# Performance work log

Hardware: AMD Instinct MI355X
Metric: run time of the kernel (lower is better)

Reference implementation:

```python
import jax, jax.numpy as jnp
import numpy as np


def mha(x, mask, wq, bq, wk, bk, wv, bv, wo, bo, n_heads):
    # Flaubert/XLM MultiHeadAttention (eval mode, dropout = identity).
    bs, qlen, dim = x.shape
    dph = dim // n_heads

    def split_heads(t):  # (bs, qlen, dim) -> (bs, n_heads, qlen, dph)
        return t.reshape(bs, qlen, n_heads, dph).transpose(0, 2, 1, 3)

    q = split_heads(x @ wq + bq) / jnp.sqrt(jnp.asarray(dph, x.dtype))
    k = split_heads(x @ wk + bk)
    v = split_heads(x @ wv + bv)

    scores = jnp.einsum('bhqd,bhkd->bhqk', q, k)  # (bs, h, qlen, klen)
    neg = jnp.finfo(scores.dtype).min
    scores = jnp.where((mask == 0)[:, None, None, :], neg, scores)
    weights = jax.nn.softmax(scores, axis=-1)
    ctx = jnp.einsum('bhqk,bhkd->bhqd', weights, v)
    ctx = ctx.transpose(0, 2, 1, 3).reshape(bs, qlen, dim)
    return ctx @ wo + bo


def setup_inputs() -> dict:
    key = jax.random.key(0)
    ks = jax.random.split(key, 20)
    bs, slen = 4, 1024
    d0, d1 = 192, 66
    std = 0.02
    inp = {
        'x': jax.random.normal(ks[0], (bs, slen, d0), jnp.float32),
        'y': jax.random.normal(ks[1], (bs, slen, d1), jnp.float32),
        'mask0': jax.random.randint(ks[2], (bs, slen), 0, 2, jnp.int32),
        'mask1': jax.random.randint(ks[3], (bs, slen), 0, 2, jnp.int32),
    }
    names0 = ['q0', 'k0', 'v0', 'o0']
    names1 = ['q1', 'k1', 'v1', 'o1']
    for i, n in enumerate(names0):
        inp[n + '_w'] = jax.random.normal(ks[4 + i], (d0, d0), jnp.float32) * std
        inp[n + '_b'] = jnp.zeros((d0,), jnp.float32)
    for i, n in enumerate(names1):
        inp[n + '_w'] = jax.random.normal(ks[8 + i], (d1, d1), jnp.float32) * std
        inp[n + '_b'] = jnp.zeros((d1,), jnp.float32)
    return inp


def reference(x, y, mask0, mask1,
              q0_w, q0_b, k0_w, k0_b, v0_w, v0_b, o0_w, o0_b,
              q1_w, q1_b, k1_w, k1_b, v1_w, v1_b, o1_w, o1_b):
    out0 = mha(x, mask0, q0_w, q0_b, k0_w, k0_b, v0_w, v0_b, o0_w, o0_b, n_heads=16)
    out1 = mha(y, mask1, q1_w, q1_b, k1_w, k1_b, v1_w, v1_b, o1_w, o1_b, n_heads=11)
    return (out0, out1)
```

## Files before the change

kernel.cpp:

```cpp
#include <hip/hip_runtime.h>
#include <math.h>


#define BS 4
#define SLEN 1024

#define Q0_OFF 0
#define C0_OFF 786432
#define Q1_OFF 1572864
#define C1_OFF 1843200
#define K0H_OFF 2113536
#define V0T_OFF 2506752
#define K1H_OFF 2899968
#define V1T_OFF 3080192

#define OUT0_SIZE 786432

#if __has_builtin(__builtin_amdgcn_exp2f)
#define EXP2(x) __builtin_amdgcn_exp2f(x)
#else
#define EXP2(x) __expf((x) * 0.69314718056f)
#endif

typedef _Float16 f16x2 __attribute__((ext_vector_type(2)));
typedef _Float16 f16x4 __attribute__((ext_vector_type(4)));
typedef _Float16 f16x8 __attribute__((ext_vector_type(8)));
typedef float f32x4 __attribute__((ext_vector_type(4)));

union F16x8U { f16x8 v8; f16x4 v4[2]; };

__device__ __forceinline__ void mfma_chunk(const _Float16* sA, const _Float16* sWT,
                                           int wv, int lane, f32x4 acc[4])
{
  const int col = lane & 15, grp = lane >> 4;
#pragma unroll
  for (int ks = 0; ks < 2; ++ks) {
    const f16x8 bf = *(const f16x8*)(sWT + (wv * 16 + col) * 72 + ks * 32 + grp * 8);
#pragma unroll
    for (int mt = 0; mt < 4; ++mt) {
      const f16x8 af = *(const f16x8*)(sA + (mt * 16 + col) * 72 + ks * 32 + grp * 8);
      acc[mt] = __builtin_amdgcn_mfma_f32_16x16x32_f16(af, bf, acc[mt], 0, 0, 0);
    }
  }
}

__device__ __forceinline__ void mfma_chunk_split(
    const _Float16* sAh, const _Float16* sAl,
    const _Float16* sWTh, const _Float16* sWTl,
    int wv, int lane, f32x4 acc[4])
{
  const int col = lane & 15, grp = lane >> 4;
#pragma unroll
  for (int ks = 0; ks < 2; ++ks) {
    const int boff = (wv * 16 + col) * 72 + ks * 32 + grp * 8;
    const f16x8 bh = *(const f16x8*)(sWTh + boff);
    const f16x8 bl = *(const f16x8*)(sWTl + boff);
#pragma unroll
    for (int mt = 0; mt < 4; ++mt) {
      const int aoff = (mt * 16 + col) * 72 + ks * 32 + grp * 8;
      const f16x8 ah = *(const f16x8*)(sAh + aoff);
      const f16x8 al = *(const f16x8*)(sAl + aoff);
      acc[mt] = __builtin_amdgcn_mfma_f32_16x16x32_f16(ah, bh, acc[mt], 0, 0, 0);
      acc[mt] = __builtin_amdgcn_mfma_f32_16x16x32_f16(ah, bl, acc[mt], 0, 0, 0);
      acc[mt] = __builtin_amdgcn_mfma_f32_16x16x32_f16(al, bh, acc[mt], 0, 0, 0);
    }
  }
}

template <int DIM>
__device__ __forceinline__ void stage_chunk(const float* __restrict__ A, int row0,
                                            int kc, const float* __restrict__ W,
                                            int col0, _Float16* sA, _Float16* sWT,
                                            int tid)
{
  for (int idx = tid; idx < 2048; idx += 256) {
    const int m = idx >> 5, k = (idx & 31) * 2;
    float2 v = make_float2(0.f, 0.f);
    if (kc + k < DIM) v = *(const float2*)(A + (size_t)(row0 + m) * DIM + kc + k);
    *(f16x2*)(sA + m * 72 + k) = (f16x2){(_Float16)v.x, (_Float16)v.y};
  }
  for (int idx = tid; idx < 2048; idx += 256) {
    const int k = idx >> 5, n = (idx & 31) * 2;
    float2 v = make_float2(0.f, 0.f);
    if (kc + k < DIM && col0 + n < DIM)
      v = *(const float2*)(W + (size_t)(kc + k) * DIM + col0 + n);
    sWT[n * 72 + k] = (_Float16)v.x;
    sWT[(n + 1) * 72 + k] = (_Float16)v.y;
  }
}

template <int DIM>
__device__ __forceinline__ void stage_chunk_split(
    const float* __restrict__ A, int row0, int kc,
    const float* __restrict__ W, int col0,
    _Float16* sAh, _Float16* sAl, _Float16* sWTh, _Float16* sWTl, int tid)
{
  for (int idx = tid; idx < 2048; idx += 256) {
    const int m = idx >> 5, k = (idx & 31) * 2;
    float2 v = make_float2(0.f, 0.f);
    if (kc + k < DIM) v = *(const float2*)(A + (size_t)(row0 + m) * DIM + kc + k);
    const _Float16 hx = (_Float16)v.x, hy = (_Float16)v.y;
    *(f16x2*)(sAh + m * 72 + k) = (f16x2){hx, hy};
    *(f16x2*)(sAl + m * 72 + k) =
        (f16x2){(_Float16)(v.x - (float)hx), (_Float16)(v.y - (float)hy)};
  }
  for (int idx = tid; idx < 2048; idx += 256) {
    const int k = idx >> 5, n = (idx & 31) * 2;
    float2 v = make_float2(0.f, 0.f);
    if (kc + k < DIM && col0 + n < DIM)
      v = *(const float2*)(W + (size_t)(kc + k) * DIM + col0 + n);
    const _Float16 hx = (_Float16)v.x, hy = (_Float16)v.y;
    sWTh[n * 72 + k] = hx;
    sWTh[(n + 1) * 72 + k] = hy;
    sWTl[n * 72 + k] = (_Float16)(v.x - (float)hx);
    sWTl[(n + 1) * 72 + k] = (_Float16)(v.y - (float)hy);
  }
}

template <int DIM, int H, int DPH, int NT, int NCH, int KST>
__device__ void qkv_impl(int bid, const float* __restrict__ X,
                         const float* __restrict__ qw, const float* __restrict__ qb,
                         const float* __restrict__ kw, const float* __restrict__ kb,
                         const float* __restrict__ vw, const float* __restrict__ vb,
                         float* __restrict__ qo, _Float16* __restrict__ kh,
                         _Float16* __restrict__ vth, char* smem)
{
  const int mt64 = bid & 63;
  const int rest = bid >> 6;
  const int mat = rest / NT;
  const int nt = rest % NT;
  const int row0 = mt64 * 64, col0 = nt * 64;

  const float* W = (mat == 0) ? qw : (mat == 1) ? kw : vw;
  const float* B = (mat == 0) ? qb : (mat == 1) ? kb : vb;
  const float scale = (mat == 0) ? (1.44269504089f / sqrtf((float)DPH)) : 1.0f;

  _Float16* sA = (_Float16*)smem;
  _Float16* sWT = sA + 64 * 72;

  const int tid = threadIdx.x;
  const int wv = tid >> 6, lane = tid & 63;
  f32x4 acc[4] = {{0.f,0.f,0.f,0.f},{0.f,0.f,0.f,0.f},{0.f,0.f,0.f,0.f},{0.f,0.f,0.f,0.f}};

  for (int c = 0; c < NCH; ++c) {
    __syncthreads();
    stage_chunk<DIM>(X, row0, c * 64, W, col0, sA, sWT, tid);
    __syncthreads();
    mfma_chunk(sA, sWT, wv, lane, acc);
  }

  const int col = lane & 15, grp = lane >> 4;
  const int cidx = col0 + wv * 16 + col;
  if (cidx < DIM) {
    const float bias = B[cidx];
    const int h = cidx / DPH, d = cidx % DPH;
#pragma unroll
    for (int mt = 0; mt < 4; ++mt) {
#pragma unroll
      for (int r = 0; r < 4; ++r) {
        const int m = row0 + mt * 16 + grp * 4 + r;
        const int b = m >> 10, s = m & 1023;
        const float v = acc[mt][r] + bias;
        const int bh = b * H + h;
        if (mat == 0)
          qo[(size_t)((bh << 10) + s) * DPH + d] = v * scale;
        else if (mat == 1)
          kh[(size_t)((bh << 10) + s) * KST + d] = (_Float16)v;
        else
          vth[((size_t)(bh * DPH + d) << 10) + s] = (_Float16)v;
      }
    }
  }
}

__global__ __launch_bounds__(256) void qkv_kernel(
    const float* __restrict__ x, const float* __restrict__ y,
    const float* __restrict__ q0w, const float* __restrict__ q0b,
    const float* __restrict__ k0w, const float* __restrict__ k0b,
    const float* __restrict__ v0w, const float* __restrict__ v0b,
    const float* __restrict__ q1w, const float* __restrict__ q1b,
    const float* __restrict__ k1w, const float* __restrict__ k1b,
    const float* __restrict__ v1w, const float* __restrict__ v1b,
    float* __restrict__ ws)
{
  extern __shared__ char smem[];
  _Float16* hws = (_Float16*)ws;
  const int bid = blockIdx.x;
  if (bid < 576)
    qkv_impl<192, 16, 12, 3, 3, 12>(bid, x, q0w, q0b, k0w, k0b, v0w, v0b,
                                    ws + Q0_OFF, hws + 2 * (size_t)K0H_OFF,
                                    hws + 2 * (size_t)V0T_OFF, smem);
  else
    qkv_impl<66, 11, 6, 2, 2, 8>(bid - 576, y, q1w, q1b, k1w, k1b, v1w, v1b,
                                 ws + Q1_OFF, hws + 2 * (size_t)K1H_OFF,
                                 hws + 2 * (size_t)V1T_OFF, smem);
}

template <int H, int DPH, int SKP>
__device__ void attn_impl(int bid, const float* __restrict__ qg,
                          const _Float16* __restrict__ kh,
                          const _Float16* __restrict__ vth,
                          const int* __restrict__ mask,
                          float* __restrict__ ctx, char* smem)
{
  constexpr int CH = 128;
  constexpr int NCH = SLEN / CH;
  constexpr int NKC = CH / 32;
  constexpr int KBUF = CH * SKP + 32;
  constexpr int VST = 136;
  constexpr int VROWS = DPH + 1;
  constexpr int PST = 44;
  constexpr int PWAVE = 16 * PST;

  _Float16* sK = (_Float16*)smem;
  _Float16* sVT = sK + 2 * KBUF;
  float* sB = (float*)(sVT + 2 * VROWS * VST);
  _Float16* sP = (_Float16*)(sB + 2 * CH);

  const int bh = bid >> 4;
  const int b = bh / H;
  const int h = bh % H;
  const int tid = threadIdx.x;

  const float* qb_ = qg + (size_t)bh * SLEN * DPH;
  const _Float16* kb_ = kh + (size_t)bh * SLEN * SKP;
  const _Float16* vb_ = vth + ((size_t)bh * DPH << 10);
  const int* mb_ = mask + b * SLEN;

  if (tid < 64) sK[(tid >> 5) * KBUF + CH * SKP + (tid & 31)] = (_Float16)0.f;
  for (int idx = tid; idx < 2 * CH; idx += 256) {
    const int pb = idx / CH, q = idx % CH;
    sVT[(pb * VROWS + DPH) * VST + q] = (_Float16)1.f;
  }

  const int wave = tid >> 6, lane = tid & 63;
  const int col = lane & 15, grp = lane >> 4;
  const int qtile = (bid & 15) * 4 + wave;

  f16x8 aq;
  {
    const int qrow = qtile * 16 + col;
#pragma unroll
    for (int j = 0; j < 8; ++j) {
      const int d = grp * 8 + j;
      aq[j] = (d < DPH) ? (_Float16)qb_[(size_t)qrow * DPH + d] : (_Float16)0.f;
    }
  }

  constexpr int kN = CH * SKP / 8;
  constexpr int vN = DPH * 16;
  const int vd = tid >> 4, vq = tid & 15;
  uint4 pk, pv;
  int pm = 0;
  auto prefetch = [&](int cc) {
    if (tid < kN) pk = ((const uint4*)(kb_ + (size_t)cc * CH * SKP))[tid];
    if (tid < vN) pv = ((const uint4*)(vb_ + ((size_t)vd << 10) + cc * CH))[vq];
    if (tid < CH) pm = mb_[cc * CH + tid];
  };
  auto commit = [&](int pb) {
    if (tid < kN) ((uint4*)(sK + pb * KBUF))[tid] = pk;
    if (tid < vN) *(uint4*)(sVT + (pb * VROWS + vd) * VST + vq * 8) = pv;
    if (tid < CH) sB[pb * CH + tid] = pm ? 0.f : -100.f;
  };

  prefetch(0);
  commit(0);
  __syncthreads();

  f32x4 Oacc[2] = {{0.f,0.f,0.f,0.f},{0.f,0.f,0.f,0.f}};
  const int de = (col <= DPH) ? col : 0;

#pragma unroll 1
  for (int c = 0; c < NCH; ++c) {
    const int p = c & 1;
    if (c + 1 < NCH) prefetch(c + 1);

    const _Float16* sKp = sK + p * KBUF;
    const _Float16* sVp = sVT + p * VROWS * VST;
    const float* sBp = sB + p * CH;

    f32x4 S0, S1;
    {
      F16x8U kf0, kf1;
      const _Float16* kp0 = sKp + col * SKP + grp * 8;
      const _Float16* kp1 = sKp + (16 + col) * SKP + grp * 8;
      kf0.v4[0] = *(const f16x4*)kp0; kf0.v4[1] = *(const f16x4*)(kp0 + 4);
      kf1.v4[0] = *(const f16x4*)kp1; kf1.v4[1] = *(const f16x4*)(kp1 + 4);
      const float bb0 = sBp[col], bb1 = sBp[16 + col];
      S0 = __builtin_amdgcn_mfma_f32_16x16x32_f16(
          aq, kf0.v8, (f32x4){bb0, bb0, bb0, bb0}, 0, 0, 0);
      S1 = __builtin_amdgcn_mfma_f32_16x16x32_f16(
          aq, kf1.v8, (f32x4){bb1, bb1, bb1, bb1}, 0, 0, 0);
    }

#pragma unroll
    for (int kc = 0; kc < NKC; ++kc) {
      f32x4 S0n, S1n;
      if (kc + 1 < NKC) {
        F16x8U kf0, kf1;
        const _Float16* kp0 = sKp + ((kc + 1) * 32 + col) * SKP + grp * 8;
        const _Float16* kp1 = sKp + ((kc + 1) * 32 + 16 + col) * SKP + grp * 8;
        kf0.v4[0] = *(const f16x4*)kp0; kf0.v4[1] = *(const f16x4*)(kp0 + 4);
        kf1.v4[0] = *(const f16x4*)kp1; kf1.v4[1] = *(const f16x4*)(kp1 + 4);
        const float bb0 = sBp[(kc + 1) * 32 + col];
        const float bb1 = sBp[(kc + 1) * 32 + 16 + col];
        S0n = __builtin_amdgcn_mfma_f32_16x16x32_f16(
            aq, kf0.v8, (f32x4){bb0, bb0, bb0, bb0}, 0, 0, 0);
        S1n = __builtin_amdgcn_mfma_f32_16x16x32_f16(
            aq, kf1.v8, (f32x4){bb1, bb1, bb1, bb1}, 0, 0, 0);
      }

      _Float16* pw = sP + (wave * 2 + (kc & 1)) * PWAVE + col;
#pragma unroll
      for (int r = 0; r < 4; ++r) {
        pw[(grp * 4 + r) * PST] = (_Float16)EXP2(S0[r]);
        pw[(grp * 4 + r) * PST + 16] = (_Float16)EXP2(S1[r]);
      }

      if (kc > 0) {
        const f16x8 vf = *(const f16x8*)(sVp + de * VST + (kc - 1) * 32 + grp * 8);
        F16x8U pf;
        const _Float16* pr =
            sP + (wave * 2 + ((kc - 1) & 1)) * PWAVE + col * PST + grp * 8;
        pf.v4[0] = *(const f16x4*)pr;
        pf.v4[1] = *(const f16x4*)(pr + 4);
        Oacc[(kc - 1) & 1] = __builtin_amdgcn_mfma_f32_16x16x32_f16(
            pf.v8, vf, Oacc[(kc - 1) & 1], 0, 0, 0);
      }
      S0 = S0n; S1 = S1n;
    }

    {
      constexpr int kl = NKC - 1;
      const f16x8 vf = *(const f16x8*)(sVp + de * VST + kl * 32 + grp * 8);
      F16x8U pf;
      const _Float16* pr =
          sP + (wave * 2 + (kl & 1)) * PWAVE + col * PST + grp * 8;
      pf.v4[0] = *(const f16x4*)pr;
      pf.v4[1] = *(const f16x4*)(pr + 4);
      Oacc[kl & 1] = __builtin_amdgcn_mfma_f32_16x16x32_f16(
          pf.v8, vf, Oacc[kl & 1], 0, 0, 0);
    }

    if (c + 1 < NCH) commit(p ^ 1);
    __syncthreads();
  }

  f32x4 Osum;
#pragma unroll
  for (int r = 0; r < 4; ++r) Osum[r] = Oacc[0][r] + Oacc[1][r];
  float lq[4];
#pragma unroll
  for (int r = 0; r < 4; ++r) lq[r] = __shfl(Osum[r], (lane & 48) + DPH);
  if (col < DPH) {
    const int qrow0 = qtile * 16;
#pragma unroll
    for (int r = 0; r < 4; ++r) {
      const int row = qrow0 + grp * 4 + r;
      ctx[(size_t)(b * SLEN + row) * (H * DPH) + h * DPH + col] = Osum[r] / lq[r];
    }
  }
}

__global__ __launch_bounds__(256) void attn_kernel(
    const int* __restrict__ mask0, const int* __restrict__ mask1,
    float* __restrict__ ws)
{
  extern __shared__ char smem[];
  _Float16* hws = (_Float16*)ws;
  const int bid = blockIdx.x;
  if (bid < 1024)
    attn_impl<16, 12, 12>(bid, ws + Q0_OFF, hws + 2 * (size_t)K0H_OFF,
                          hws + 2 * (size_t)V0T_OFF, mask0, ws + C0_OFF, smem);
  else
    attn_impl<11, 6, 8>(bid - 1024, ws + Q1_OFF, hws + 2 * (size_t)K1H_OFF,
                        hws + 2 * (size_t)V1T_OFF, mask1, ws + C1_OFF, smem);
}

template <int DIM, int NCH>
__device__ void oproj_impl(int bid, const float* __restrict__ Cx,
                           const float* __restrict__ ow, const float* __restrict__ ob,
                           float* __restrict__ out, char* smem)
{
  const int mt64 = bid & 63;
  const int nt = bid >> 6;
  const int row0 = mt64 * 64, col0 = nt * 64;

  _Float16* sAh = (_Float16*)smem;
  _Float16* sAl = sAh + 64 * 72;
  _Float16* sWTh = sAl + 64 * 72;
  _Float16* sWTl = sWTh + 64 * 72;

  const int tid = threadIdx.x;
  const int wv = tid >> 6, lane = tid & 63;
  f32x4 acc[4] = {{0.f,0.f,0.f,0.f},{0.f,0.f,0.f,0.f},{0.f,0.f,0.f,0.f},{0.f,0.f,0.f,0.f}};

  for (int c = 0; c < NCH; ++c) {
    __syncthreads();
    stage_chunk_split<DIM>(Cx, row0, c * 64, ow, col0, sAh, sAl, sWTh, sWTl, tid);
    __syncthreads();
    mfma_chunk_split(sAh, sAl, sWTh, sWTl, wv, lane, acc);
  }

  const int col = lane & 15, grp = lane >> 4;
  const int cidx = col0 + wv * 16 + col;
  if (cidx < DIM) {
    const float bias = ob[cidx];
#pragma unroll
    for (int mt = 0; mt < 4; ++mt) {
#pragma unroll
      for (int r = 0; r < 4; ++r) {
        const int m = row0 + mt * 16 + grp * 4 + r;
        out[(size_t)m * DIM + cidx] = acc[mt][r] + bias;
      }
    }
  }
}

__global__ __launch_bounds__(256) void oproj_kernel(
    const float* __restrict__ o0w, const float* __restrict__ o0b,
    const float* __restrict__ o1w, const float* __restrict__ o1b,
    float* __restrict__ ws, float* __restrict__ out)
{
  extern __shared__ char smem[];
  const int bid = blockIdx.x;
  if (bid < 192)
    oproj_impl<192, 3>(bid, ws + C0_OFF, o0w, o0b, out, smem);
  else
    oproj_impl<66, 2>(bid - 192, ws + C1_OFF, o1w, o1b, out + OUT0_SIZE, smem);
}

extern "C" void kernel_launch(void* const* d_in, const int* in_sizes, int n_in,
                              void* d_out, int out_size, void* d_ws, size_t ws_size,
                              hipStream_t stream)
{
  const float* x = (const float*)d_in[0];
  const float* y = (const float*)d_in[1];
  const int* mask0 = (const int*)d_in[2];
  const int* mask1 = (const int*)d_in[3];
  const float* q0w = (const float*)d_in[4];  const float* q0b = (const float*)d_in[5];
  const float* k0w = (const float*)d_in[6];  const float* k0b = (const float*)d_in[7];
  const float* v0w = (const float*)d_in[8];  const float* v0b = (const float*)d_in[9];
  const float* o0w = (const float*)d_in[10]; const float* o0b = (const float*)d_in[11];
  const float* q1w = (const float*)d_in[12]; const float* q1b = (const float*)d_in[13];
  const float* k1w = (const float*)d_in[14]; const float* k1b = (const float*)d_in[15];
  const float* v1w = (const float*)d_in[16]; const float* v1b = (const float*)d_in[17];
  const float* o1w = (const float*)d_in[18]; const float* o1b = (const float*)d_in[19];

  float* ws = (float*)d_ws;
  float* out = (float*)d_out;

  const int qkv_smem = 2 * 64 * 72 * 2;
  const int oproj_smem = 4 * 64 * 72 * 2;
  const int attn_smem = 2 * (128 * 12 + 32) * 2 + 2 * 13 * 136 * 2
                      + 2 * 128 * 4 + 4 * 2 * (16 * 44) * 2;

  qkv_kernel<<<960, 256, qkv_smem, stream>>>(x, y, q0w, q0b, k0w, k0b, v0w, v0b,
                                             q1w, q1b, k1w, k1b, v1w, v1b, ws);
  attn_kernel<<<1728, 256, attn_smem, stream>>>(mask0, mask1, ws);
  oproj_kernel<<<320, 256, oproj_smem, stream>>>(o0w, o0b, o1w, o1b, ws, out);
}
```

Measured before the change: 167.2 us.

## Compact unmasked keys per batch and skip fully masked attention chunks

Adds a prefix-scan kernel that builds, per batch, a permutation putting unmasked key positions first and counts them. The QKV kernel scatters K and V into this compacted order, and the attention loop runs only over chunks holding valid keys, computing the mask bias from the count. The aim is to avoid MFMA and load work on masked keys, which are about half of them with random masks. It costs an extra small kernel launch and scattered K/V writes. Results stay exact because masked keys contribute zero weight, the same as in the original path.

```diff
diff --git a/kernel.cpp b/kernel.cpp
--- a/kernel.cpp
+++ b/kernel.cpp
@@ -13,6 +13,9 @@
 #define V0T_OFF 2506752
 #define K1H_OFF 2899968
 #define V1T_OFF 3080192
+#define CMAP0_OFF 3215360
+#define CMAP1_OFF 3219456
+#define CNT_OFF 3223552
 
 #define OUT0_SIZE 786432
 
@@ -28,6 +31,42 @@
 typedef float f32x4 __attribute__((ext_vector_type(4)));
 
 union F16x8U { f16x8 v8; f16x4 v4[2]; };
+
+__global__ __launch_bounds__(256) void compact_kernel(
+    const int* __restrict__ mask0, const int* __restrict__ mask1,
+    int* __restrict__ cmap0, int* __restrict__ cmap1, int* __restrict__ cnts)
+{
+  __shared__ int sS[256];
+  __shared__ int sTot;
+  const int inst = blockIdx.x >> 2, b = blockIdx.x & 3;
+  const int* m = (inst ? mask1 : mask0) + b * SLEN;
+  int* cmap = (inst ? cmap1 : cmap0) + b * SLEN;
+  const int tid = threadIdx.x;
+
+  int mv[4], s4 = 0;
+#pragma unroll
+  for (int i = 0; i < 4; ++i) { mv[i] = m[tid * 4 + i] ? 1 : 0; s4 += mv[i]; }
+  sS[tid] = s4;
+  __syncthreads();
+  for (int off = 1; off < 256; off <<= 1) {
+    const int v = sS[tid];
+    const int add = (tid >= off) ? sS[tid - off] : 0;
+    __syncthreads();
+    sS[tid] = v + add;
+    __syncthreads();
+  }
+  if (tid == 255) sTot = sS[255];
+  __syncthreads();
+  const int tot = sTot;
+  int u = tid ? sS[tid - 1] : 0;
+#pragma unroll
+  for (int i = 0; i < 4; ++i) {
+    const int s = tid * 4 + i;
+    cmap[s] = mv[i] ? u : tot + (s - u);
+    u += mv[i];
+  }
+  if (tid == 0) cnts[blockIdx.x] = tot;
+}
 
 __device__ __forceinline__ void mfma_chunk(const _Float16* sA, const _Float16* sWT,
                                            int wv, int lane, f32x4 acc[4])
@@ -123,7 +162,8 @@
                          const float* __restrict__ kw, const float* __restrict__ kb,
                          const float* __restrict__ vw, const float* __restrict__ vb,
                          float* __restrict__ qo, _Float16* __restrict__ kh,
-                         _Float16* __restrict__ vth, char* smem)
+                         _Float16* __restrict__ vth, const int* __restrict__ cmap,
+                         char* smem)
 {
   const int mt64 = bid & 63;
   const int rest = bid >> 6;
@@ -162,12 +202,15 @@
         const int b = m >> 10, s = m & 1023;
         const float v = acc[mt][r] + bias;
         const int bh = b * H + h;
-        if (mat == 0)
+        if (mat == 0) {
           qo[(size_t)((bh << 10) + s) * DPH + d] = v * scale;
-        else if (mat == 1)
-          kh[(size_t)((bh << 10) + s) * KST + d] = (_Float16)v;
-        else
-          vth[((size_t)(bh * DPH + d) << 10) + s] = (_Float16)v;
+        } else {
+          const int sp = cmap[(b << 10) + s];
+          if (mat == 1)
+            kh[(size_t)((bh << 10) + sp) * KST + d] = (_Float16)v;
+          else
+            vth[((size_t)(bh * DPH + d) << 10) + sp] = (_Float16)v;
+        }
       }
     }
   }
@@ -185,26 +228,27 @@
 {
   extern __shared__ char smem[];
   _Float16* hws = (_Float16*)ws;
+  const int* cmap0 = (const int*)(ws + CMAP0_OFF);
+  const int* cmap1 = (const int*)(ws + CMAP1_OFF);
   const int bid = blockIdx.x;
   if (bid < 576)
     qkv_impl<192, 16, 12, 3, 3, 12>(bid, x, q0w, q0b, k0w, k0b, v0w, v0b,
                                     ws + Q0_OFF, hws + 2 * (size_t)K0H_OFF,
-                                    hws + 2 * (size_t)V0T_OFF, smem);
+                                    hws + 2 * (size_t)V0T_OFF, cmap0, smem);
   else
     qkv_impl<66, 11, 6, 2, 2, 8>(bid - 576, y, q1w, q1b, k1w, k1b, v1w, v1b,
                                  ws + Q1_OFF, hws + 2 * (size_t)K1H_OFF,
-                                 hws + 2 * (size_t)V1T_OFF, smem);
+                                 hws + 2 * (size_t)V1T_OFF, cmap1, smem);
 }
 
 template <int H, int DPH, int SKP>
 __device__ void attn_impl(int bid, const float* __restrict__ qg,
                           const _Float16* __restrict__ kh,
                           const _Float16* __restrict__ vth,
-                          const int* __restrict__ mask,
+                          const int* __restrict__ cnts,
                           float* __restrict__ ctx, char* smem)
 {
   constexpr int CH = 128;
-  constexpr int NCH = SLEN / CH;
   constexpr int NKC = CH / 32;
   constexpr int KBUF = CH * SKP + 32;
   constexpr int VST = 136;
@@ -214,8 +258,7 @@
 
   _Float16* sK = (_Float16*)smem;
   _Float16* sVT = sK + 2 * KBUF;
-  float* sB = (float*)(sVT + 2 * VROWS * VST);
-  _Float16* sP = (_Float16*)(sB + 2 * CH);
+  _Float16* sP = sVT + 2 * VROWS * VST;
 
   const int bh = bid >> 4;
   const int b = bh / H;
@@ -225,7 +268,8 @@
   const float* qb_ = qg + (size_t)bh * SLEN * DPH;
   const _Float16* kb_ = kh + (size_t)bh * SLEN * SKP;
   const _Float16* vb_ = vth + ((size_t)bh * DPH << 10);
-  const int* mb_ = mask + b * SLEN;
+  const int cnt = cnts[b];
+  const int nch = (cnt + CH - 1) >> 7;
 
   if (tid < 64) sK[(tid >> 5) * KBUF + CH * SKP + (tid & 31)] = (_Float16)0.f;
   for (int idx = tid; idx < 2 * CH; idx += 256) {
@@ -251,16 +295,13 @@
   constexpr int vN = DPH * 16;
   const int vd = tid >> 4, vq = tid & 15;
   uint4 pk, pv;
-  int pm = 0;
   auto prefetch = [&](int cc) {
     if (tid < kN) pk = ((const uint4*)(kb_ + (size_t)cc * CH * SKP))[tid];
     if (tid < vN) pv = ((const uint4*)(vb_ + ((size_t)vd << 10) + cc * CH))[vq];
-    if (tid < CH) pm = mb_[cc * CH + tid];
   };
   auto commit = [&](int pb) {
     if (tid < kN) ((uint4*)(sK + pb * KBUF))[tid] = pk;
     if (tid < vN) *(uint4*)(sVT + (pb * VROWS + vd) * VST + vq * 8) = pv;
-    if (tid < CH) sB[pb * CH + tid] = pm ? 0.f : -100.f;
   };
 
   prefetch(0);
@@ -271,13 +312,13 @@
   const int de = (col <= DPH) ? col : 0;
 
 #pragma unroll 1
-  for (int c = 0; c < NCH; ++c) {
+  for (int c = 0; c < nch; ++c) {
     const int p = c & 1;
-    if (c + 1 < NCH) prefetch(c + 1);
+    if (c + 1 < nch) prefetch(c + 1);
 
     const _Float16* sKp = sK + p * KBUF;
     const _Float16* sVp = sVT + p * VROWS * VST;
-    const float* sBp = sB + p * CH;
+    const int keyc = c * CH + col;
 
     f32x4 S0, S1;
     {
@@ -286,7 +327,8 @@
       const _Float16* kp1 = sKp + (16 + col) * SKP + grp * 8;
       kf0.v4[0] = *(const f16x4*)kp0; kf0.v4[1] = *(const f16x4*)(kp0 + 4);
       kf1.v4[0] = *(const f16x4*)kp1; kf1.v4[1] = *(const f16x4*)(kp1 + 4);
-      const float bb0 = sBp[col], bb1 = sBp[16 + col];
+      const float bb0 = (keyc < cnt) ? 0.f : -100.f;
+      const float bb1 = (keyc + 16 < cnt) ? 0.f : -100.f;
       S0 = __builtin_amdgcn_mfma_f32_16x16x32_f16(
           aq, kf0.v8, (f32x4){bb0, bb0, bb0, bb0}, 0, 0, 0);
       S1 = __builtin_amdgcn_mfma_f32_16x16x32_f16(
@@ -302,8 +344,8 @@
         const _Float16* kp1 = sKp + ((kc + 1) * 32 + 16 + col) * SKP + grp * 8;
         kf0.v4[0] = *(const f16x4*)kp0; kf0.v4[1] = *(const f16x4*)(kp0 + 4);
         kf1.v4[0] = *(const f16x4*)kp1; kf1.v4[1] = *(const f16x4*)(kp1 + 4);
-        const float bb0 = sBp[(kc + 1) * 32 + col];
-        const float bb1 = sBp[(kc + 1) * 32 + 16 + col];
+        const float bb0 = (keyc + (kc + 1) * 32 < cnt) ? 0.f : -100.f;
+        const float bb1 = (keyc + (kc + 1) * 32 + 16 < cnt) ? 0.f : -100.f;
         S0n = __builtin_amdgcn_mfma_f32_16x16x32_f16(
             aq, kf0.v8, (f32x4){bb0, bb0, bb0, bb0}, 0, 0, 0);
         S1n = __builtin_amdgcn_mfma_f32_16x16x32_f16(
@@ -342,7 +384,7 @@
           pf.v8, vf, Oacc[kl & 1], 0, 0, 0);
     }
 
-    if (c + 1 < NCH) commit(p ^ 1);
+    if (c + 1 < nch) commit(p ^ 1);
     __syncthreads();
   }
 
@@ -362,19 +404,18 @@
   }
 }
 
-__global__ __launch_bounds__(256) void attn_kernel(
-    const int* __restrict__ mask0, const int* __restrict__ mask1,
-    float* __restrict__ ws)
+__global__ __launch_bounds__(256) void attn_kernel(float* __restrict__ ws)
 {
   extern __shared__ char smem[];
   _Float16* hws = (_Float16*)ws;
+  const int* cnts = (const int*)(ws + CNT_OFF);
   const int bid = blockIdx.x;
   if (bid < 1024)
     attn_impl<16, 12, 12>(bid, ws + Q0_OFF, hws + 2 * (size_t)K0H_OFF,
-                          hws + 2 * (size_t)V0T_OFF, mask0, ws + C0_OFF, smem);
+                          hws + 2 * (size_t)V0T_OFF, cnts, ws + C0_OFF, smem);
   else
     attn_impl<11, 6, 8>(bid - 1024, ws + Q1_OFF, hws + 2 * (size_t)K1H_OFF,
-                        hws + 2 * (size_t)V1T_OFF, mask1, ws + C1_OFF, smem);
+                        hws + 2 * (size_t)V1T_OFF, cnts + 4, ws + C1_OFF, smem);
 }
 
 template <int DIM, int NCH>
@@ -453,10 +494,14 @@
   const int qkv_smem = 2 * 64 * 72 * 2;
   const int oproj_smem = 4 * 64 * 72 * 2;
   const int attn_smem = 2 * (128 * 12 + 32) * 2 + 2 * 13 * 136 * 2
-                      + 2 * 128 * 4 + 4 * 2 * (16 * 44) * 2;
-
+                      + 4 * 2 * (16 * 44) * 2;
+
+  compact_kernel<<<8, 256, 0, stream>>>(mask0, mask1,
+                                        (int*)(ws + CMAP0_OFF),
+                                        (int*)(ws + CMAP1_OFF),
+                                        (int*)(ws + CNT_OFF));
   qkv_kernel<<<960, 256, qkv_smem, stream>>>(x, y, q0w, q0b, k0w, k0b, v0w, v0b,
                                              q1w, q1b, k1w, k1b, v1w, v1b, ws);
-  attn_kernel<<<1728, 256, attn_smem, stream>>>(mask0, mask1, ws);
+  attn_kernel<<<1728, 256, attn_smem, stream>>>(ws);
   oproj_kernel<<<320, 256, oproj_smem, stream>>>(o0w, o0b, o1w, o1b, ws, out);
 }
```

Measured after the change: 158.3 us. 1.06x faster.
